# Performance work log

Measured on AMD Instinct MI355X. Metric: run time of the kernel, lower is better.

## Reference

```python
import jax, jax.numpy as jnp
import numpy as np

DIM = 768
NUM_HEADS = 12
SMALLEST_RATIO = 0.25
LARGEST_RATIO = 1.0


def setup_inputs() -> dict:
    key = jax.random.key(0)
    k0, k1, k2 = jax.random.split(key, 3)
    B, N = 4, 2048
    x = jax.random.normal(k0, (B, N, DIM), dtype=jnp.float32)
    Wqkv = jax.random.normal(k1, (3 * DIM, DIM), dtype=jnp.float32) * 0.02
    bqkv = jnp.zeros((3 * DIM,), dtype=jnp.float32)
    Wproj = jax.random.normal(k2, (DIM, DIM), dtype=jnp.float32) * 0.02
    bproj = jnp.zeros((DIM,), dtype=jnp.float32)
    return {"x": x, "Wqkv": Wqkv, "bqkv": bqkv, "Wproj": Wproj, "bproj": bproj, "ratio": 1}


def reference(x, Wqkv, bqkv, Wproj, bproj, ratio):
    dc = int(ratio * DIM)
    # dynamic slimmable-width slicing: smallest/largest ratio take leading block,
    # intermediate ratios take trailing block
    if ratio == SMALLEST_RATIO or ratio == LARGEST_RATIO:
        wq, bq = Wqkv[: dc * 3, :dc], bqkv[: dc * 3]
        wp, bp = Wproj[:dc, :dc], bproj[:dc]
    else:
        wq, bq = Wqkv[-dc * 3 :, -dc:], bqkv[-dc * 3 :]
        wp, bp = Wproj[-dc:, -dc:], bproj[-dc:]
    B, N, C = x.shape
    hd = C // NUM_HEADS
    scale = (DIM // NUM_HEADS) ** -0.5  # set at init from full dim, not sliced C
    qkv = x @ wq.T + bq                               # [B, N, 3C]
    qkv = qkv.reshape(B, N, 3, NUM_HEADS, hd).transpose(2, 0, 3, 1, 4)  # [3,B,H,N,hd]
    q, k, v = qkv[0], qkv[1], qkv[2]
    attn = jax.nn.softmax(jnp.einsum("bhqd,bhkd->bhqk", q, k) * scale, axis=-1)
    out = jnp.einsum("bhqk,bhkd->bhqd", attn, v)      # [B,H,N,hd]
    out = out.transpose(0, 2, 1, 3).reshape(B, N, C)
    return out @ wp.T + bp
```

## Files before the change

kernel.cpp:

```cpp
#include <hip/hip_runtime.h>

typedef __bf16 bf16x8 __attribute__((ext_vector_type(8)));
typedef __bf16 bf16x2 __attribute__((ext_vector_type(2)));
typedef float  f32x4  __attribute__((ext_vector_type(4)));
typedef float  f32x16 __attribute__((ext_vector_type(16)));
typedef unsigned short u16;
typedef unsigned u32x2 __attribute__((ext_vector_type(2)));
typedef unsigned u32x4 __attribute__((ext_vector_type(4)));

__device__ __forceinline__ u16 f2bf(float f) {
  return __builtin_bit_cast(u16, (__bf16)f);
}
__device__ __forceinline__ unsigned pack2(float lo, float hi) {
  bf16x2 t;
  t[0] = (__bf16)lo; t[1] = (__bf16)hi;
  return __builtin_bit_cast(unsigned, t);
}

#define GLOAD16(g, l) __builtin_amdgcn_global_load_lds( \
    (__attribute__((address_space(1))) void*)(void*)(g), \
    (__attribute__((address_space(3))) void*)(l), 16, 0, 0)

#define QSCALE 0.18033688011112042f

__global__ __launch_bounds__(256) void cvt_all(
    const float* __restrict__ x, const float* __restrict__ wq,
    const float* __restrict__ wp, unsigned* __restrict__ xb,
    unsigned* __restrict__ wqb, unsigned* __restrict__ wpb) {
  int i = blockIdx.x * 256 + threadIdx.x;
  const float* src;
  unsigned* dst;
  if (i < 786432) {
    src = x; dst = xb;
  } else if (i < 786432 + 221184) {
    src = wq; dst = wqb; i -= 786432;
  } else {
    src = wp; dst = wpb; i -= 786432 + 221184;
  }
  const float4* s = (const float4*)src + 2 * (size_t)i;
  float4 a = s[0], b = s[1];
  u32x4 o = {pack2(a.x, a.y), pack2(a.z, a.w), pack2(b.x, b.y), pack2(b.z, b.w)};
  *((u32x4*)dst + i) = o;
}

template<int EPI>
__global__ __launch_bounds__(256) void gemm_tn(
    const u16* __restrict__ A, const u16* __restrict__ B,
    const float* __restrict__ bias, float* __restrict__ outF,
    u16* __restrict__ qws, u16* __restrict__ kws, u16* __restrict__ vtws,
    int M, int N, int K) {
  __shared__ __align__(16) u16 As[8192];
  __shared__ __align__(16) u16 Bs[8192];
  const int tid = threadIdx.x;
  const int ln = tid & 63, wv = tid >> 6;
  const int wr = wv >> 1, wc = wv & 1;
  const int m0 = blockIdx.x * 128, n0 = blockIdx.y * 128;

  f32x4 acc[4][4] = {};

  const int c0 = tid, c1 = tid + 256;
  const int r0 = c0 >> 2, kc0 = ((c0 & 3) ^ ((r0 >> 1) & 3)) * 8;
  const int r1 = c1 >> 2, kc1 = ((c1 & 3) ^ ((r1 >> 1) & 3)) * 8;
  const u16* ag0 = A + (size_t)(m0 + r0) * K + kc0;
  const u16* ag1 = A + (size_t)(m0 + r1) * K + kc1;
  const u16* bg0 = B + (size_t)(n0 + r0) * K + kc0;
  const u16* bg1 = B + (size_t)(n0 + r1) * K + kc1;

  GLOAD16(ag0, As + wv * 512);
  GLOAD16(ag1, As + 2048 + wv * 512);
  GLOAD16(bg0, Bs + wv * 512);
  GLOAD16(bg1, Bs + 2048 + wv * 512);
  __syncthreads();

  int cur = 0;
  for (int k0 = 0; k0 < K; k0 += 32) {
    const int nxt = cur ^ 1;
    if (k0 + 32 < K) {
      GLOAD16(ag0 + k0 + 32, As + nxt * 4096 + wv * 512);
      GLOAD16(ag1 + k0 + 32, As + nxt * 4096 + 2048 + wv * 512);
      GLOAD16(bg0 + k0 + 32, Bs + nxt * 4096 + wv * 512);
      GLOAD16(bg1 + k0 + 32, Bs + nxt * 4096 + 2048 + wv * 512);
    }
    const u16* ab = As + cur * 4096;
    const u16* bb = Bs + cur * 4096;
    bf16x8 af[4], bfr[4];
#pragma unroll
    for (int i = 0; i < 4; ++i) {
      int ra = wr * 64 + i * 16 + (ln & 15);
      af[i] = *(const bf16x8*)(ab + ra * 32 + (((ln >> 4) ^ ((ra >> 1) & 3)) * 8));
      int rb = wc * 64 + i * 16 + (ln & 15);
      bfr[i] = *(const bf16x8*)(bb + rb * 32 + (((ln >> 4) ^ ((rb >> 1) & 3)) * 8));
    }
#pragma unroll
    for (int i = 0; i < 4; ++i)
#pragma unroll
      for (int j = 0; j < 4; ++j)
        acc[i][j] = __builtin_amdgcn_mfma_f32_16x16x32_bf16(af[i], bfr[j], acc[i][j], 0, 0, 0);
    __syncthreads();
    cur = nxt;
  }

  if (EPI == 1) {
#pragma unroll
    for (int j = 0; j < 4; ++j) {
      int col = n0 + wc * 64 + j * 16 + (ln & 15);
      float bj = bias[col];
#pragma unroll
      for (int i = 0; i < 4; ++i) {
        int mr = m0 + wr * 64 + i * 16 + ((ln >> 4) << 2);
#pragma unroll
        for (int r = 0; r < 4; ++r)
          outF[(size_t)(mr + r) * N + col] = acc[i][j][r] + bj;
      }
    }
  } else {
    const int s = n0 / 768;
#pragma unroll
    for (int j = 0; j < 4; ++j) {
      int col = n0 + wc * 64 + j * 16 + (ln & 15);
      float bj = bias[col];
      int ns = col - s * 768;
      int h = ns >> 6, d = ns & 63;
#pragma unroll
      for (int i = 0; i < 4; ++i) {
        int m = m0 + wr * 64 + i * 16 + ((ln >> 4) << 2);
        int b = m >> 11, iseq = m & 2047;
        size_t bh = (size_t)(b * 12 + h);
        if (s == 0) {
#pragma unroll
          for (int r = 0; r < 4; ++r)
            qws[(bh * 2048 + iseq + r) * 64 + d] = f2bf((acc[i][j][r] + bj) * QSCALE);
        } else if (s == 1) {
#pragma unroll
          for (int r = 0; r < 4; ++r)
            kws[(bh * 2048 + iseq + r) * 64 + d] = f2bf(acc[i][j][r] + bj);
        } else {
          u32x2 pk = {pack2(acc[i][j][0] + bj, acc[i][j][1] + bj),
                      pack2(acc[i][j][2] + bj, acc[i][j][3] + bj)};
          *(u32x2*)(vtws + ((size_t)bh * 64 + (iseq >> 5)) * 2048 +
                    ((iseq >> 3) & 3) * 512 + (size_t)d * 8 + (iseq & 7)) = pk;
        }
      }
    }
  }
}

__global__ __launch_bounds__(256, 2) void attn_fa(
    const u16* __restrict__ qws, const u16* __restrict__ kws,
    const u16* __restrict__ vtws, u16* __restrict__ aows) {
  __shared__ __align__(16) u16 SM[40960];
  const int tid = threadIdx.x, ln = tid & 63, wv = tid >> 6;
  const int lq = ln & 31, hi = ln >> 5;

  const int flat = blockIdx.y * 64 + blockIdx.x;
  const int xcd = flat & 7, jj = flat >> 3;
  const int bh = xcd * 6 + (jj % 6);
  const int q0 = (jj / 6) * 32;

  const int kv0 = wv * 512;
  const size_t kbase = (size_t)bh * 2048 * 64;

  bf16x8 qf[4];
  {
    const u16* qp = qws + kbase + (size_t)(q0 + lq) * 64 + hi * 8;
#pragma unroll
    for (int dc = 0; dc < 4; ++dc) qf[dc] = *(const bf16x8*)(qp + dc * 16);
  }

  const f32x16 zc = {};
  f32x16 o0 = {}, o1 = {};
  float lsum = 0.f;

  int koff[4], voff[2];
#pragma unroll
  for (int dc = 0; dc < 4; ++dc)
    koff[dc] = lq * 64 + (((dc * 2 + hi) ^ (lq & 7)) * 8);
#pragma unroll
  for (int c = 0; c < 2; ++c)
    voff[c] = (c * 2 + hi) * 512 + lq * 8;

  const int r0 = ln >> 3;
  const int chs = ((ln & 7) ^ r0) * 8;
  const int pib = (r0 & 3) | ((r0 & 4) << 1);
  const u16* kgb = kws + kbase + (size_t)(kv0 + pib) * 64 + chs;
  const u16* vg  = vtws + ((size_t)bh * 64 + (kv0 >> 5)) * 2048 + (size_t)ln * 8;
  u16* Kw = SM + wv * 10240;
  u16* Vw = Kw + 4096;
  const int dst = ln * 8;

#define STAGE_K(buf, t) do { \
    GLOAD16(kgb + (size_t)(t) * 2048,        Kw + (buf) * 2048 + dst); \
    GLOAD16(kgb + (size_t)(t) * 2048 + 256,  Kw + (buf) * 2048 + 512 + dst); \
    GLOAD16(kgb + (size_t)(t) * 2048 + 1024, Kw + (buf) * 2048 + 1024 + dst); \
    GLOAD16(kgb + (size_t)(t) * 2048 + 1280, Kw + (buf) * 2048 + 1536 + dst); \
  } while (0)
#define STAGE_V(buf, t) do { \
    GLOAD16(vg + (size_t)(t) * 2048,        Vw + (buf) * 2048 + dst); \
    GLOAD16(vg + (size_t)(t) * 2048 + 512,  Vw + (buf) * 2048 + 512 + dst); \
    GLOAD16(vg + (size_t)(t) * 2048 + 1024, Vw + (buf) * 2048 + 1024 + dst); \
    GLOAD16(vg + (size_t)(t) * 2048 + 1536, Vw + (buf) * 2048 + 1536 + dst); \
  } while (0)

#define QKEXP(PW0, PW1) do { \
    const u16* kb_ = Kw + kq * 2048; \
    bf16x8 kf0 = *(const bf16x8*)(kb_ + koff[0]); \
    f32x16 s_ = __builtin_amdgcn_mfma_f32_32x32x16_bf16(kf0, qf[0], zc, 0, 0, 0); \
    bf16x8 kf1 = *(const bf16x8*)(kb_ + koff[1]); \
    s_ = __builtin_amdgcn_mfma_f32_32x32x16_bf16(kf1, qf[1], s_, 0, 0, 0); \
    bf16x8 kf2 = *(const bf16x8*)(kb_ + koff[2]); \
    s_ = __builtin_amdgcn_mfma_f32_32x32x16_bf16(kf2, qf[2], s_, 0, 0, 0); \
    bf16x8 kf3 = *(const bf16x8*)(kb_ + koff[3]); \
    s_ = __builtin_amdgcn_mfma_f32_32x32x16_bf16(kf3, qf[3], s_, 0, 0, 0); \
    float a_ = 0.f, b_ = 0.f; \
    _Pragma("unroll") \
    for (int r = 0; r < 16; r += 2) { \
      float e0 = __builtin_amdgcn_exp2f(s_[r]);     s_[r] = e0;     a_ += e0; \
      float e1 = __builtin_amdgcn_exp2f(s_[r + 1]); s_[r + 1] = e1; b_ += e1; \
    } \
    lsum += a_ + b_; \
    PW0 = (u32x4){pack2(s_[0], s_[1]),   pack2(s_[2], s_[3]), \
                  pack2(s_[4], s_[5]),   pack2(s_[6], s_[7])}; \
    PW1 = (u32x4){pack2(s_[8], s_[9]),   pack2(s_[10], s_[11]), \
                  pack2(s_[12], s_[13]), pack2(s_[14], s_[15])}; \
  } while (0)

#define PVSTEP(PR0, PR1) do { \
    const u16* vb_ = Vw + vp * 2048; \
    bf16x8 va0 = *(const bf16x8*)(vb_ + voff[0]); \
    bf16x8 vb0 = *(const bf16x8*)(vb_ + voff[0] + 256); \
    bf16x8 va1 = *(const bf16x8*)(vb_ + voff[1]); \
    bf16x8 vb1 = *(const bf16x8*)(vb_ + voff[1] + 256); \
    o0 = __builtin_amdgcn_mfma_f32_32x32x16_bf16(va0, __builtin_bit_cast(bf16x8, PR0), o0, 0, 0, 0); \
    o1 = __builtin_amdgcn_mfma_f32_32x32x16_bf16(vb0, __builtin_bit_cast(bf16x8, PR0), o1, 0, 0, 0); \
    o0 = __builtin_amdgcn_mfma_f32_32x32x16_bf16(va1, __builtin_bit_cast(bf16x8, PR1), o0, 0, 0, 0); \
    o1 = __builtin_amdgcn_mfma_f32_32x32x16_bf16(vb1, __builtin_bit_cast(bf16x8, PR1), o1, 0, 0, 0); \
  } while (0)

#define BODY(PR0, PR1, PW0, PW1, DOSTAGE) do { \
    asm volatile("s_waitcnt vmcnt(4)" ::: "memory"); \
    if (DOSTAGE) { STAGE_K(ks, t + 2); STAGE_V(vs, t + 2); } \
    QKEXP(PW0, PW1); \
    PVSTEP(PR0, PR1); \
    kq ^= 1; ks ^= 1; vp = (vp == 2) ? 0 : vp + 1; vs = (vs == 2) ? 0 : vs + 1; \
    ++t; \
  } while (0)

  u32x4 pA0, pA1, pB0, pB1;

  STAGE_K(0, 0);
  STAGE_V(0, 0);
  STAGE_K(1, 1);
  STAGE_V(1, 1);
  asm volatile("s_waitcnt vmcnt(12)" ::: "memory");
  int t = 0, kq = 0, ks = 0, vp = 0, vs = 2;
  QKEXP(pA0, pA1);
  kq = 1;

  for (int i = 0; i < 7; ++i) {
    BODY(pA0, pA1, pB0, pB1, 1);
    BODY(pB0, pB1, pA0, pA1, 1);
  }
  BODY(pA0, pA1, pB0, pB1, 0);
  asm volatile("s_waitcnt vmcnt(0)" ::: "memory");
  PVSTEP(pB0, pB1);
#undef BODY
#undef PVSTEP
#undef QKEXP
#undef STAGE_V
#undef STAGE_K

  float lg = lsum + __shfl_xor(lsum, 32);

  __syncthreads();
  float* ex = (float*)SM;
  if (wv > 0) {
    float* w = ex + (wv - 1) * 2112 + ln;
#pragma unroll
    for (int r = 0; r < 16; ++r) {
      w[r * 64]        = o0[r];
      w[(16 + r) * 64] = o1[r];
    }
    ex[6336 + (wv - 1) * 64 + ln] = lg;
  }
  __syncthreads();
  if (wv == 0) {
#pragma unroll
    for (int w2 = 0; w2 < 3; ++w2) {
      const float* w = ex + w2 * 2112 + ln;
#pragma unroll
      for (int r = 0; r < 16; ++r) {
        o0[r] += w[r * 64];
        o1[r] += w[(16 + r) * 64];
      }
      lg += ex[6336 + w2 * 64 + ln];
    }
    const float rl = 1.0f / lg;
    const int b = bh / 12, h = bh % 12;
    u16* orow = aows + (size_t)(b * 2048 + q0 + lq) * 768 + h * 64;
#pragma unroll
    for (int t2 = 0; t2 < 4; ++t2) {
      u32x2 pk0 = {pack2(o0[4 * t2 + 0] * rl, o0[4 * t2 + 1] * rl),
                   pack2(o0[4 * t2 + 2] * rl, o0[4 * t2 + 3] * rl)};
      u32x2 pk1 = {pack2(o1[4 * t2 + 0] * rl, o1[4 * t2 + 1] * rl),
                   pack2(o1[4 * t2 + 2] * rl, o1[4 * t2 + 3] * rl)};
      *(u32x2*)(orow + t2 * 8 + 4 * hi)      = pk0;
      *(u32x2*)(orow + 32 + t2 * 8 + 4 * hi) = pk1;
    }
  }
}

extern "C" void kernel_launch(void* const* d_in, const int* in_sizes, int n_in,
                              void* d_out, int out_size, void* d_ws, size_t ws_size,
                              hipStream_t stream) {
  const float* x     = (const float*)d_in[0];
  const float* Wqkv  = (const float*)d_in[1];
  const float* bqkv  = (const float*)d_in[2];
  const float* Wproj = (const float*)d_in[3];
  const float* bproj = (const float*)d_in[4];
  float* out = (float*)d_out;

  u16* xb   = (u16*)d_ws;
  u16* wqb  = xb  + 6291456;
  u16* wpb  = wqb + 1769472;
  u16* qws  = wpb + 589824;
  u16* kws  = qws + 6291456;
  u16* vtws = kws + 6291456;
  u16* aows = vtws + 6291456;

  cvt_all<<<4224, 256, 0, stream>>>(x, Wqkv, Wproj,
                                    (unsigned*)xb, (unsigned*)wqb, (unsigned*)wpb);

  gemm_tn<0><<<dim3(64, 18), 256, 0, stream>>>(xb, wqb, bqkv, nullptr,
                                               qws, kws, vtws, 8192, 2304, 768);
  attn_fa<<<dim3(64, 48), 256, 0, stream>>>(qws, kws, vtws, aows);
  gemm_tn<1><<<dim3(64, 6), 256, 0, stream>>>(aows, wpb, bproj, out,
                                              nullptr, nullptr, nullptr,
                                              8192, 768, 768);
}
```

Before: 157.5 us.

## Store K in MFMA fragment layout and load K/V directly into registers

The QKV projection epilogue now writes K in a pre-swizzled fragment layout that matches the MFMA operand order, so each lane can load its K fragment straight from global memory. The attention kernel drops the LDS staging pipeline (global_load_lds with triple/double buffering and waitcnt juggling) in favour of register prefetch of the next K/V tile, and shrinks shared memory to only the cross-wave reduction buffer. Occupancy target rises from 2 to 4 blocks per CU. The trade is losing explicit multi-stage latency hiding: only one tile is prefetched into registers, and the kernel relies on higher occupancy and the cache to cover global load latency.

```diff
diff --git a/kernel.cpp b/kernel.cpp
--- a/kernel.cpp
+++ b/kernel.cpp
@@ -121,6 +121,7 @@
       float bj = bias[col];
       int ns = col - s * 768;
       int h = ns >> 6, d = ns & 63;
+      int dc = d >> 4, hid = (d >> 3) & 1, jd = d & 7;
 #pragma unroll
       for (int i = 0; i < 4; ++i) {
         int m = m0 + wr * 64 + i * 16 + ((ln >> 4) << 2);
@@ -132,8 +133,12 @@
             qws[(bh * 2048 + iseq + r) * 64 + d] = f2bf((acc[i][j][r] + bj) * QSCALE);
         } else if (s == 1) {
 #pragma unroll
-          for (int r = 0; r < 4; ++r)
-            kws[(bh * 2048 + iseq + r) * 64 + d] = f2bf(acc[i][j][r] + bj);
+          for (int r = 0; r < 4; ++r) {
+            int row = iseq + r, rr = row & 31;
+            int pl = (rr & ~12) | ((rr & 4) << 1) | ((rr & 8) >> 1);
+            kws[((size_t)bh * 64 + (row >> 5)) * 2048 + dc * 512 +
+                (hid * 32 + pl) * 8 + jd] = f2bf(acc[i][j][r] + bj);
+          }
         } else {
           u32x2 pk = {pack2(acc[i][j][0] + bj, acc[i][j][1] + bj),
                       pack2(acc[i][j][2] + bj, acc[i][j][3] + bj)};
@@ -145,10 +150,10 @@
   }
 }
 
-__global__ __launch_bounds__(256, 2) void attn_fa(
-    const u16* __restrict__ qws, const u16* __restrict__ kws,
+__global__ __launch_bounds__(256, 4) void attn_fa(
+    const u16* __restrict__ qws, const u16* __restrict__ kfws,
     const u16* __restrict__ vtws, u16* __restrict__ aows) {
-  __shared__ __align__(16) u16 SM[40960];
+  __shared__ float EX[6528];
   const int tid = threadIdx.x, ln = tid & 63, wv = tid >> 6;
   const int lq = ln & 31, hi = ln >> 5;
 
@@ -171,128 +176,78 @@
   f32x16 o0 = {}, o1 = {};
   float lsum = 0.f;
 
-  int koff[4], voff[2];
-#pragma unroll
-  for (int dc = 0; dc < 4; ++dc)
-    koff[dc] = lq * 64 + (((dc * 2 + hi) ^ (lq & 7)) * 8);
-#pragma unroll
-  for (int c = 0; c < 2; ++c)
-    voff[c] = (c * 2 + hi) * 512 + lq * 8;
-
-  const int r0 = ln >> 3;
-  const int chs = ((ln & 7) ^ r0) * 8;
-  const int pib = (r0 & 3) | ((r0 & 4) << 1);
-  const u16* kgb = kws + kbase + (size_t)(kv0 + pib) * 64 + chs;
-  const u16* vg  = vtws + ((size_t)bh * 64 + (kv0 >> 5)) * 2048 + (size_t)ln * 8;
-  u16* Kw = SM + wv * 10240;
-  u16* Vw = Kw + 4096;
-  const int dst = ln * 8;
-
-#define STAGE_K(buf, t) do { \
-    GLOAD16(kgb + (size_t)(t) * 2048,        Kw + (buf) * 2048 + dst); \
-    GLOAD16(kgb + (size_t)(t) * 2048 + 256,  Kw + (buf) * 2048 + 512 + dst); \
-    GLOAD16(kgb + (size_t)(t) * 2048 + 1024, Kw + (buf) * 2048 + 1024 + dst); \
-    GLOAD16(kgb + (size_t)(t) * 2048 + 1280, Kw + (buf) * 2048 + 1536 + dst); \
+  const u16* kfb = kfws + ((size_t)bh * 64 + (kv0 >> 5)) * 2048 + ln * 8;
+  const u16* vfb = vtws + ((size_t)bh * 64 + (kv0 >> 5)) * 2048;
+  const int vA0 = hi * 512 + lq * 8;
+  const int vB0 = vA0 + 256;
+  const int vA1 = vA0 + 1024;
+  const int vB1 = vA1 + 256;
+
+  bf16x8 kf0, kf1, kf2, kf3, va0, vb0, va1, vb1;
+
+#define LOADK(t) do { const u16* kp_ = kfb + (size_t)(t) * 2048; \
+    kf0 = *(const bf16x8*)(kp_);        kf1 = *(const bf16x8*)(kp_ + 512); \
+    kf2 = *(const bf16x8*)(kp_ + 1024); kf3 = *(const bf16x8*)(kp_ + 1536); \
   } while (0)
-#define STAGE_V(buf, t) do { \
-    GLOAD16(vg + (size_t)(t) * 2048,        Vw + (buf) * 2048 + dst); \
-    GLOAD16(vg + (size_t)(t) * 2048 + 512,  Vw + (buf) * 2048 + 512 + dst); \
-    GLOAD16(vg + (size_t)(t) * 2048 + 1024, Vw + (buf) * 2048 + 1024 + dst); \
-    GLOAD16(vg + (size_t)(t) * 2048 + 1536, Vw + (buf) * 2048 + 1536 + dst); \
+#define LOADV(t) do { const u16* vp_ = vfb + (size_t)(t) * 2048; \
+    va0 = *(const bf16x8*)(vp_ + vA0); vb0 = *(const bf16x8*)(vp_ + vB0); \
+    va1 = *(const bf16x8*)(vp_ + vA1); vb1 = *(const bf16x8*)(vp_ + vB1); \
   } while (0)
 
-#define QKEXP(PW0, PW1) do { \
-    const u16* kb_ = Kw + kq * 2048; \
-    bf16x8 kf0 = *(const bf16x8*)(kb_ + koff[0]); \
-    f32x16 s_ = __builtin_amdgcn_mfma_f32_32x32x16_bf16(kf0, qf[0], zc, 0, 0, 0); \
-    bf16x8 kf1 = *(const bf16x8*)(kb_ + koff[1]); \
-    s_ = __builtin_amdgcn_mfma_f32_32x32x16_bf16(kf1, qf[1], s_, 0, 0, 0); \
-    bf16x8 kf2 = *(const bf16x8*)(kb_ + koff[2]); \
-    s_ = __builtin_amdgcn_mfma_f32_32x32x16_bf16(kf2, qf[2], s_, 0, 0, 0); \
-    bf16x8 kf3 = *(const bf16x8*)(kb_ + koff[3]); \
-    s_ = __builtin_amdgcn_mfma_f32_32x32x16_bf16(kf3, qf[3], s_, 0, 0, 0); \
-    float a_ = 0.f, b_ = 0.f; \
-    _Pragma("unroll") \
-    for (int r = 0; r < 16; r += 2) { \
-      float e0 = __builtin_amdgcn_exp2f(s_[r]);     s_[r] = e0;     a_ += e0; \
-      float e1 = __builtin_amdgcn_exp2f(s_[r + 1]); s_[r + 1] = e1; b_ += e1; \
-    } \
-    lsum += a_ + b_; \
-    PW0 = (u32x4){pack2(s_[0], s_[1]),   pack2(s_[2], s_[3]), \
-                  pack2(s_[4], s_[5]),   pack2(s_[6], s_[7])}; \
-    PW1 = (u32x4){pack2(s_[8], s_[9]),   pack2(s_[10], s_[11]), \
-                  pack2(s_[12], s_[13]), pack2(s_[14], s_[15])}; \
-  } while (0)
-
-#define PVSTEP(PR0, PR1) do { \
-    const u16* vb_ = Vw + vp * 2048; \
-    bf16x8 va0 = *(const bf16x8*)(vb_ + voff[0]); \
-    bf16x8 vb0 = *(const bf16x8*)(vb_ + voff[0] + 256); \
-    bf16x8 va1 = *(const bf16x8*)(vb_ + voff[1]); \
-    bf16x8 vb1 = *(const bf16x8*)(vb_ + voff[1] + 256); \
-    o0 = __builtin_amdgcn_mfma_f32_32x32x16_bf16(va0, __builtin_bit_cast(bf16x8, PR0), o0, 0, 0, 0); \
-    o1 = __builtin_amdgcn_mfma_f32_32x32x16_bf16(vb0, __builtin_bit_cast(bf16x8, PR0), o1, 0, 0, 0); \
-    o0 = __builtin_amdgcn_mfma_f32_32x32x16_bf16(va1, __builtin_bit_cast(bf16x8, PR1), o0, 0, 0, 0); \
-    o1 = __builtin_amdgcn_mfma_f32_32x32x16_bf16(vb1, __builtin_bit_cast(bf16x8, PR1), o1, 0, 0, 0); \
-  } while (0)
-
-#define BODY(PR0, PR1, PW0, PW1, DOSTAGE) do { \
-    asm volatile("s_waitcnt vmcnt(4)" ::: "memory"); \
-    if (DOSTAGE) { STAGE_K(ks, t + 2); STAGE_V(vs, t + 2); } \
-    QKEXP(PW0, PW1); \
-    PVSTEP(PR0, PR1); \
-    kq ^= 1; ks ^= 1; vp = (vp == 2) ? 0 : vp + 1; vs = (vs == 2) ? 0 : vs + 1; \
-    ++t; \
-  } while (0)
-
-  u32x4 pA0, pA1, pB0, pB1;
-
-  STAGE_K(0, 0);
-  STAGE_V(0, 0);
-  STAGE_K(1, 1);
-  STAGE_V(1, 1);
-  asm volatile("s_waitcnt vmcnt(12)" ::: "memory");
-  int t = 0, kq = 0, ks = 0, vp = 0, vs = 2;
-  QKEXP(pA0, pA1);
-  kq = 1;
-
-  for (int i = 0; i < 7; ++i) {
-    BODY(pA0, pA1, pB0, pB1, 1);
-    BODY(pB0, pB1, pA0, pA1, 1);
-  }
-  BODY(pA0, pA1, pB0, pB1, 0);
-  asm volatile("s_waitcnt vmcnt(0)" ::: "memory");
-  PVSTEP(pB0, pB1);
-#undef BODY
-#undef PVSTEP
-#undef QKEXP
-#undef STAGE_V
-#undef STAGE_K
+  LOADK(0);
+  LOADV(0);
+  for (int t = 0; t < 16; ++t) {
+    f32x16 s = __builtin_amdgcn_mfma_f32_32x32x16_bf16(kf0, qf[0], zc, 0, 0, 0);
+    s = __builtin_amdgcn_mfma_f32_32x32x16_bf16(kf1, qf[1], s, 0, 0, 0);
+    s = __builtin_amdgcn_mfma_f32_32x32x16_bf16(kf2, qf[2], s, 0, 0, 0);
+    s = __builtin_amdgcn_mfma_f32_32x32x16_bf16(kf3, qf[3], s, 0, 0, 0);
+    if (t + 1 < 16) LOADK(t + 1);
+
+    float a = 0.f, b2 = 0.f;
+#pragma unroll
+    for (int r = 0; r < 16; r += 2) {
+      float e0 = __builtin_amdgcn_exp2f(s[r]);     s[r] = e0;     a  += e0;
+      float e1 = __builtin_amdgcn_exp2f(s[r + 1]); s[r + 1] = e1; b2 += e1;
+    }
+    lsum += a + b2;
+    u32x4 P0 = {pack2(s[0], s[1]),   pack2(s[2], s[3]),
+                pack2(s[4], s[5]),   pack2(s[6], s[7])};
+    u32x4 P1 = {pack2(s[8], s[9]),   pack2(s[10], s[11]),
+                pack2(s[12], s[13]), pack2(s[14], s[15])};
+    bf16x8 p0 = __builtin_bit_cast(bf16x8, P0);
+    bf16x8 p1 = __builtin_bit_cast(bf16x8, P1);
+
+    o0 = __builtin_amdgcn_mfma_f32_32x32x16_bf16(va0, p0, o0, 0, 0, 0);
+    o1 = __builtin_amdgcn_mfma_f32_32x32x16_bf16(vb0, p0, o1, 0, 0, 0);
+    o0 = __builtin_amdgcn_mfma_f32_32x32x16_bf16(va1, p1, o0, 0, 0, 0);
+    o1 = __builtin_amdgcn_mfma_f32_32x32x16_bf16(vb1, p1, o1, 0, 0, 0);
+    if (t + 1 < 16) LOADV(t + 1);
+  }
+#undef LOADV
+#undef LOADK
 
   float lg = lsum + __shfl_xor(lsum, 32);
 
-  __syncthreads();
-  float* ex = (float*)SM;
   if (wv > 0) {
-    float* w = ex + (wv - 1) * 2112 + ln;
+    float* w = EX + (wv - 1) * 2112 + ln;
 #pragma unroll
     for (int r = 0; r < 16; ++r) {
       w[r * 64]        = o0[r];
       w[(16 + r) * 64] = o1[r];
     }
-    ex[6336 + (wv - 1) * 64 + ln] = lg;
+    EX[6336 + (wv - 1) * 64 + ln] = lg;
   }
   __syncthreads();
   if (wv == 0) {
 #pragma unroll
     for (int w2 = 0; w2 < 3; ++w2) {
-      const float* w = ex + w2 * 2112 + ln;
+      const float* w = EX + w2 * 2112 + ln;
 #pragma unroll
       for (int r = 0; r < 16; ++r) {
         o0[r] += w[r * 64];
         o1[r] += w[(16 + r) * 64];
       }
-      lg += ex[6336 + w2 * 64 + ln];
+      lg += EX[6336 + w2 * 64 + ln];
     }
     const float rl = 1.0f / lg;
     const int b = bh / 12, h = bh % 12;
```

After: 144.3 us. 1.09x faster.
